# Optimization experiments

Measured on AMD Instinct MI355X. Metric: run time of the kernel, lower is better.

The kernel has to match this reference:

```python
import jax, jax.numpy as jnp
import numpy as np

NEG = -1e30       # log-space 'zero'
KD_FACTOR = 0.5   # self.kd_factor
KD_TEMP = 1.0     # self.kd_temp is never set in the original __init__; use 1.0
BLANK = 0         # torch CTCLoss default blank id


def ctc_loss(logits, targets, ilens, olens):
    """CTC negative log-likelihood, sum-reduced / B (matches builtin path:
    log_softmax + nn.CTCLoss(reduction='sum', zero_infinity=True) / batch).
    logits: [B,T,C]; targets: [B,L] label ids (no blanks); ilens, olens: [B]."""
    B, T, C = logits.shape
    L = targets.shape[1]
    S = 2 * L + 1
    lp = jax.nn.log_softmax(logits, axis=-1)                     # [B,T,C]
    # extended label sequence: blank, y1, blank, y2, ..., blank  -> [B,S]
    ext = jnp.zeros((B, S), dtype=targets.dtype).at[:, 1::2].set(targets)
    prev2 = jnp.pad(ext, ((0, 0), (2, 0)))[:, :S]
    allow2 = (ext != BLANK) & (ext != prev2) & (jnp.arange(S)[None, :] >= 2)
    # per-frame emission log-probs of extended labels: [T,B,S]
    emit = jnp.take_along_axis(lp, jnp.broadcast_to(ext[:, None, :], (B, T, S)), axis=2)
    emit = jnp.transpose(emit, (1, 0, 2))
    alpha0 = (jnp.full((B, S), NEG, dtype=lp.dtype)
              .at[:, 0].set(emit[0, :, 0])
              .at[:, 1].set(emit[0, :, 1]))

    def step(alpha, xs):
        e_t, t = xs
        s1 = jnp.pad(alpha, ((0, 0), (1, 0)), constant_values=NEG)[:, :S]
        s2 = jnp.where(allow2, jnp.pad(alpha, ((0, 0), (2, 0)), constant_values=NEG)[:, :S], NEG)
        m = jnp.maximum(jnp.maximum(alpha, s1), s2)
        new = m + jnp.log(jnp.exp(alpha - m) + jnp.exp(s1 - m) + jnp.exp(s2 - m)) + e_t
        # freeze alpha past each sample's input length -> alpha at t = ilen-1
        new = jnp.where((t < ilens)[:, None], new, alpha)
        return new, None

    alpha, _ = jax.lax.scan(step, alpha0, (emit[1:], jnp.arange(1, T)))
    end = 2 * olens                                              # last blank index
    bidx = jnp.arange(B)
    ll = jnp.logaddexp(alpha[bidx, end], alpha[bidx, end - 1])
    loss = -ll
    loss = jnp.where(loss > 1e20, 0.0, loss)                     # zero_infinity
    return loss.sum() / B


def kd_loss(logits, soft_logits, hlens):
    """Vectorized form of the per-sample ragged KD loop:
    sum_b -(softmax(soft[b,:h]/T) * log_softmax(logits[b,:h]/T)).sum() / B."""
    B, T, _ = logits.shape
    p = jax.nn.softmax(soft_logits / KD_TEMP, axis=-1)
    logq = jax.nn.log_softmax(logits / KD_TEMP, axis=-1)
    cxe = -(p * logq).sum(-1)                                    # [B,T]
    mask = jnp.arange(T)[None, :] < hlens[:, None]
    return jnp.where(mask, cxe, 0.0).sum() / B


def setup_inputs() -> dict:
    key = jax.random.key(0)
    k1, k2, k3, k4, k5, k6 = jax.random.split(key, 6)
    B, T, E, V, L = 16, 512, 512, 5000, 64
    hs_pad = jax.random.normal(k1, (B, T, E), jnp.float32)
    soft_logits = jax.random.normal(k2, (B, T, V), jnp.float32)
    W = jax.random.normal(k3, (E, V), jnp.float32) * 0.02
    b = jnp.zeros((V,), jnp.float32)
    hlens = jax.random.randint(k4, (B,), 300, T + 1)             # T >= 2L+1 guaranteed
    targets = jax.random.randint(k5, (B, L), 1, V)               # no blank labels
    olens = jax.random.randint(k6, (B,), 32, L + 1)
    return {"hs_pad": hs_pad, "soft_logits": soft_logits, "W": W, "b": b,
            "hlens": hlens, "targets": targets, "olens": olens}


def reference(hs_pad, soft_logits, W, b, hlens, targets, olens):
    # ctc_lo(F.dropout(hs_pad, p=0.0)) -> plain linear projection
    logits = hs_pad @ W + b                                      # [B,T,V]
    loss_ctc = ctc_loss(logits, targets, hlens, olens)
    loss_kd = kd_loss(logits, soft_logits, hlens)
    return KD_FACTOR * loss_kd + (1.0 - KD_FACTOR) * loss_ctc
```

## Files before the change

kernel.cpp:

```cpp
#include <hip/hip_runtime.h>
#include <math.h>

#define LOG2E 1.4426950408889634f
#define LN2 0.6931471805599453f

constexpr int B_ = 16;
constexpr int T_ = 512;
constexpr int E_ = 512;
constexpr int V_ = 5000;
constexpr int VP_ = 5120;
constexpr int CB_ = VP_ / 128;
constexpr int L_ = 64;
constexpr int S_ = 2 * L_ + 1;
constexpr int SP_ = 132;
constexpr int CLDS_STRIDE = 132;

typedef __attribute__((ext_vector_type(8))) short bf16x8;
typedef __attribute__((ext_vector_type(4))) float f32x4;

#define GLOAD_LDS16(g, l)                                                              \
  __builtin_amdgcn_global_load_lds((const __attribute__((address_space(1))) void*)(g), \
                                   (__attribute__((address_space(3))) void*)(l), 16, 0, 0)

__device__ __forceinline__ unsigned short f2bf(float x) {
  unsigned int u = __float_as_uint(x);
  unsigned int r = (u + 0x7fffu + ((u >> 16) & 1u)) >> 16;
  return (unsigned short)r;
}
__device__ __forceinline__ float bf2f(unsigned int lo16) {
  return __uint_as_float(lo16 << 16);
}

__device__ __forceinline__ float hexp2(float x) { return __builtin_amdgcn_exp2f(x); }
__device__ __forceinline__ float hlog2(float x) { return __builtin_amdgcn_logf(x); }

__device__ __forceinline__ float dpp_shr1_zero(float v) {
  int s = __float_as_int(v);
  int bc = __builtin_amdgcn_update_dpp(0, s, 0x142, 0xF, 0xF, false);
  int r = __builtin_amdgcn_update_dpp(bc, s, 0x111, 0xF, 0xF, false);
  return __int_as_float(r);
}

template <int CTRL>
__device__ __forceinline__ float dpp_mv(float v) {
  int s = __float_as_int(v);
  return __int_as_float(__builtin_amdgcn_update_dpp(s, s, CTRL, 0xF, 0xF, false));
}

__device__ __forceinline__ float blockReduceF(float v, bool is_max, volatile float* red) {
  int tid = threadIdx.x, lane = tid & 63, wid = tid >> 6;
#pragma unroll
  for (int off = 32; off > 0; off >>= 1) {
    float o = __shfl_down(v, off, 64);
    v = is_max ? fmaxf(v, o) : (v + o);
  }
  __syncthreads();
  if (lane == 0) red[wid] = v;
  __syncthreads();
  float r = red[0];
#pragma unroll
  for (int w = 1; w < 4; ++w) r = is_max ? fmaxf(r, (float)red[w]) : (r + (float)red[w]);
  return r;
}

__global__ __launch_bounds__(256) void convA(const float* __restrict__ X,
                                             unsigned short* __restrict__ Y, int n4) {
  int i = blockIdx.x * 256 + threadIdx.x;
  if (i >= n4) return;
  float4 v = ((const float4*)X)[i];
  ushort4 o;
  o.x = f2bf(v.x); o.y = f2bf(v.y); o.z = f2bf(v.z); o.w = f2bf(v.w);
  ((ushort4*)Y)[i] = o;
}

__global__ __launch_bounds__(256) void convW(const float* __restrict__ W,
                                             unsigned short* __restrict__ Wt) {
  __shared__ float tile[32][33];
  int n0 = blockIdx.x * 32, k0 = blockIdx.y * 32;
  int tid = threadIdx.x;
  int tx = tid & 31, ty = tid >> 5;
#pragma unroll
  for (int p = 0; p < 4; ++p) {
    int k = k0 + ty + p * 8, n = n0 + tx;
    tile[ty + p * 8][tx] = (n < V_) ? W[(size_t)k * V_ + n] : 0.0f;
  }
  __syncthreads();
#pragma unroll
  for (int p = 0; p < 4; ++p) {
    int n = n0 + ty + p * 8, k = k0 + tx;
    Wt[(size_t)n * E_ + k] = f2bf(tile[tx][ty + p * 8]);
  }
}

__global__ __launch_bounds__(256) void gemm_fused(const unsigned short* __restrict__ A,
                                                  const unsigned short* __restrict__ Wt,
                                                  const float* __restrict__ bias,
                                                  const float* __restrict__ soft,
                                                  const int* __restrict__ targets,
                                                  float* __restrict__ part,
                                                  float* __restrict__ lraw) {
  __shared__ __align__(16) char smem[128 * CLDS_STRIDE * 2];
  __shared__ int tgt[64];
  unsigned short* As = (unsigned short*)smem;
  unsigned short* Bs = As + 128 * 32;
  unsigned short* Clds = (unsigned short*)smem;

  int tid = threadIdx.x;
  int l = tid & 63, wid = tid >> 6;
  int lane15 = l & 15, lhalf = l >> 4;
  int wr = wid >> 1, wc = wid & 1;
  int bn = blockIdx.x * 128;
  int bm = blockIdx.y * 128;
  int bidx = bm >> 9;
  if (tid < 64) tgt[tid] = targets[bidx * L_ + tid];

  f32x4 acc[4][4] = {};

  int srow = l >> 2;
  int scol = (l & 3) * 8;
  for (int k0 = 0; k0 < E_; k0 += 32) {
#pragma unroll
    for (int i = 0; i < 2; ++i) {
      int rb = wid * 32 + i * 16;
      GLOAD_LDS16(A + (size_t)(bm + rb + srow) * E_ + k0 + scol, &As[rb * 32]);
      GLOAD_LDS16(Wt + (size_t)(bn + rb + srow) * E_ + k0 + scol, &Bs[rb * 32]);
    }
    __syncthreads();
    bf16x8 af[4], bf[4];
#pragma unroll
    for (int m = 0; m < 4; ++m)
      af[m] = *(const bf16x8*)&As[(wr * 64 + m * 16 + lane15) * 32 + lhalf * 8];
#pragma unroll
    for (int n = 0; n < 4; ++n)
      bf[n] = *(const bf16x8*)&Bs[(wc * 64 + n * 16 + lane15) * 32 + lhalf * 8];
#pragma unroll
    for (int m = 0; m < 4; ++m)
#pragma unroll
      for (int n = 0; n < 4; ++n)
        acc[m][n] = __builtin_amdgcn_mfma_f32_16x16x32_bf16(af[m], bf[n], acc[m][n], 0, 0, 0);
    __syncthreads();
  }

#pragma unroll
  for (int n = 0; n < 4; ++n) {
    int cl = wc * 64 + n * 16 + lane15;
    int col = bn + cl;
    float bv = (col < V_) ? bias[col] : 0.0f;
#pragma unroll
    for (int m = 0; m < 4; ++m) {
      int r0 = wr * 64 + m * 16 + lhalf * 4;
#pragma unroll
      for (int j = 0; j < 4; ++j)
        Clds[(r0 + j) * CLDS_STRIDE + cl] = f2bf(acc[m][n][j] + bv);
    }
  }
  __syncthreads();

  int r = tid >> 1, ch = tid & 1;
  const float* srp = soft + (size_t)(bm + r) * V_ + bn + ch * 64;
  const unsigned short* clr = Clds + r * CLDS_STRIDE + ch * 64;
  float pl = 0.f, ps = 0.f, pd = 0.f;
  if (bn + 128 <= V_) {
#pragma unroll 4
    for (int i = 0; i < 16; ++i) {
      float4 sv = *(const float4*)(srp + i * 4);
      ushort4 lv = *(const ushort4*)(clr + i * 4);
      float l0 = bf2f(lv.x), l1 = bf2f(lv.y), l2 = bf2f(lv.z), l3 = bf2f(lv.w);
      pl += hexp2(l0 * LOG2E) + hexp2(l1 * LOG2E) + hexp2(l2 * LOG2E) + hexp2(l3 * LOG2E);
      float e0 = hexp2(sv.x * LOG2E), e1 = hexp2(sv.y * LOG2E);
      float e2 = hexp2(sv.z * LOG2E), e3 = hexp2(sv.w * LOG2E);
      ps += (e0 + e1) + (e2 + e3);
      pd = fmaf(e0, l0, fmaf(e1, l1, fmaf(e2, l2, fmaf(e3, l3, pd))));
    }
  } else {
    for (int i = 0; i < 64; ++i) {
      int col = bn + ch * 64 + i;
      if (col < V_) {
        float s = srp[i];
        float lv = bf2f(clr[i]);
        pl += hexp2(lv * LOG2E);
        float e = hexp2(s * LOG2E);
        ps += e;
        pd = fmaf(e, lv, pd);
      }
    }
  }
  pl += __shfl_xor(pl, 1, 64);
  ps += __shfl_xor(ps, 1, 64);
  pd += __shfl_xor(pd, 1, 64);
  if (ch == 0) {
    float* pp = part + ((size_t)(bm + r) * CB_ + blockIdx.x) * 3;
    pp[0] = pl; pp[1] = ps; pp[2] = pd;
  }

  if (tid < 128) {
    int row = tid;
    const unsigned short* cr = Clds + row * CLDS_STRIDE;
    float* lr = lraw + (size_t)(bm + row) * SP_;
#pragma unroll 1
    for (int s = 0; s < S_; ++s) {
      int c = (s & 1) ? tgt[s >> 1] : 0;
      int cc = c - bn;
      if (cc >= 0 && cc < 128) lr[s] = bf2f(cr[cc]);
    }
  }
}

__global__ __launch_bounds__(256) void finalize(const float* __restrict__ part,
                                                const float* __restrict__ lraw,
                                                const int* __restrict__ hlens,
                                                float* __restrict__ cxe,
                                                float* __restrict__ emit) {
  int row = blockIdx.x * 4 + (threadIdx.x >> 6);
  int l = threadIdx.x & 63;
  int bidx = row >> 9, t = row & (T_ - 1);
  const float* pp = part + (size_t)row * CB_ * 3;
  float sl = 0.f, ss = 0.f, sd = 0.f;
  if (l < CB_) { sl = pp[l * 3]; ss = pp[l * 3 + 1]; sd = pp[l * 3 + 2]; }
#pragma unroll
  for (int off = 32; off > 0; off >>= 1) {
    sl += __shfl_xor(sl, off, 64);
    ss += __shfl_xor(ss, off, 64);
    sd += __shfl_xor(sd, off, 64);
  }
  float lse = hlog2(sl) * LN2;
  if (l == 0) cxe[row] = (t < hlens[bidx]) ? (lse - sd / ss) : 0.0f;

  const float* lr = lraw + (size_t)row * SP_;
  float e0 = (lr[l] - lse) * LOG2E;
  float e1 = (lr[l + 64] - lse) * LOG2E;
  float e2 = (l == 0) ? (lr[128] - lse) * LOG2E : -3e38f;
  float m = fmaxf(fmaxf(e0, e1), e2);
#pragma unroll
  for (int off = 32; off > 0; off >>= 1) m = fmaxf(m, __shfl_xor(m, off, 64));
  float* er = emit + (size_t)row * SP_;
  er[l] = hexp2(e0 - m);
  er[l + 64] = hexp2(e1 - m);
  if (l == 0) {
    er[128] = hexp2(e2 - m);
    er[130] = m;
  }
}

__device__ __forceinline__ void pstep(float& a0, float& a1, float& a2, float allowf,
                                      float e0, float e1, float e2) {
  float ua1 = dpp_shr1_zero(a1);
  float n0 = (a0 + ua1) * e0;
  float n1 = fmaf(ua1, allowf, a0 + a1) * e1;
  float n2 = (a2 + a1) * e2;
  a0 = n0; a1 = n1; a2 = n2;
}

__device__ __forceinline__ void renorm(float& a0, float& a1, float& a2, float& shift,
                                       int lane) {
  float m = fmaxf(a0, a1);
  m = (lane == 63) ? fmaxf(m, a2) : m;
  m = fmaxf(m, dpp_mv<0xB1>(m));
  m = fmaxf(m, dpp_mv<0x4E>(m));
  m = fmaxf(m, dpp_mv<0x124>(m));
  m = fmaxf(m, dpp_mv<0x128>(m));
  m = fmaxf(m, __shfl_xor(m, 16, 64));
  m = fmaxf(m, __shfl_xor(m, 32, 64));
  m = fmaxf(m, 1e-35f);
  float rs = __builtin_amdgcn_rcpf(m) * 281474976710656.0f;
  a0 *= rs; a1 *= rs; a2 *= rs;
  shift -= hlog2(rs);
}

__global__ __launch_bounds__(64) void ctc_fwd(const float* __restrict__ emit,
                                              const int* __restrict__ hlens,
                                              const int* __restrict__ targets,
                                              const int* __restrict__ olens,
                                              float* __restrict__ ctc_out) {
  int b = blockIdx.x;
  int l = threadIdx.x;
  const float* Eb = emit + (size_t)b * T_ * SP_;
  float allowf = 0.f;
  if (l >= 1) allowf = (targets[b * L_ + l] != targets[b * L_ + l - 1]) ? 1.0f : 0.0f;

  float a0, a1, a2, shift;
  {
    float2 e01 = *(const float2*)(Eb + 2 * l);
    float4 x = *(const float4*)(Eb + 128);
    a0 = (l == 0) ? e01.x : 0.0f;
    a1 = (l == 0) ? e01.y : 0.0f;
    a2 = 0.0f;
    shift = x.z;
  }
  int ilen = hlens[b];

#define LDE(tt) (*(const float2*)(Eb + (size_t)(tt) * SP_ + 2 * l))
#define LDX(tt) (*(const float4*)(Eb + (size_t)(tt) * SP_ + 128))

  float2 c0 = LDE(1), c1 = LDE(2), c2 = LDE(3), c3 = LDE(4);
  float2 c4 = LDE(5), c5 = LDE(6), c6 = LDE(7), c7 = LDE(8);
  float4 x0 = LDX(1), x1 = LDX(2), x2 = LDX(3), x3 = LDX(4);
  float4 x4 = LDX(5), x5 = LDX(6), x6 = LDX(7), x7 = LDX(8);

  int t = 1;
  for (; t + 7 <= ilen - 1; t += 8) {
    float2 p0 = LDE(t + 8), p1 = LDE(t + 9), p2 = LDE(t + 10), p3 = LDE(t + 11);
    float2 p4 = LDE(t + 12), p5 = LDE(t + 13), p6 = LDE(t + 14), p7 = LDE(t + 15);
    float4 q0 = LDX(t + 8), q1 = LDX(t + 9), q2 = LDX(t + 10), q3 = LDX(t + 11);
    float4 q4 = LDX(t + 12), q5 = LDX(t + 13), q6 = LDX(t + 14), q7 = LDX(t + 15);
    pstep(a0, a1, a2, allowf, c0.x, c0.y, x0.x);
    pstep(a0, a1, a2, allowf, c1.x, c1.y, x1.x);
    pstep(a0, a1, a2, allowf, c2.x, c2.y, x2.x);
    pstep(a0, a1, a2, allowf, c3.x, c3.y, x3.x);
    pstep(a0, a1, a2, allowf, c4.x, c4.y, x4.x);
    pstep(a0, a1, a2, allowf, c5.x, c5.y, x5.x);
    pstep(a0, a1, a2, allowf, c6.x, c6.y, x6.x);
    pstep(a0, a1, a2, allowf, c7.x, c7.y, x7.x);
    shift += ((x0.z + x1.z) + (x2.z + x3.z)) + ((x4.z + x5.z) + (x6.z + x7.z));
    renorm(a0, a1, a2, shift, l);
    c0 = p0; c1 = p1; c2 = p2; c3 = p3; c4 = p4; c5 = p5; c6 = p6; c7 = p7;
    x0 = q0; x1 = q1; x2 = q2; x3 = q3; x4 = q4; x5 = q5; x6 = q6; x7 = q7;
  }
  int rem = ilen - t;
  if (rem > 0) { pstep(a0, a1, a2, allowf, c0.x, c0.y, x0.x); shift += x0.z; }
  if (rem > 1) { pstep(a0, a1, a2, allowf, c1.x, c1.y, x1.x); shift += x1.z; }
  if (rem > 2) { pstep(a0, a1, a2, allowf, c2.x, c2.y, x2.x); shift += x2.z; }
  if (rem > 3) { pstep(a0, a1, a2, allowf, c3.x, c3.y, x3.x); shift += x3.z; }
  if (rem > 4) { pstep(a0, a1, a2, allowf, c4.x, c4.y, x4.x); shift += x4.z; }
  if (rem > 5) { pstep(a0, a1, a2, allowf, c5.x, c5.y, x5.x); shift += x5.z; }
  if (rem > 6) { pstep(a0, a1, a2, allowf, c6.x, c6.y, x6.x); shift += x6.z; }
#undef LDE
#undef LDX

  int end = 2 * olens[b];
  float aE = (end == 128) ? __shfl(a2, 63, 64) : __shfl(a0, end >> 1, 64);
  float aE1 = __shfl(a1, (end >> 1) - 1, 64);
  if (l == 0) {
    float p = aE + aE1;
    float ll = (hlog2(p) + shift) * LN2;
    float loss = -ll;
    if (!(loss <= 1e20f)) loss = 0.0f;
    ctc_out[b] = loss;
  }
}

__global__ __launch_bounds__(256) void final_reduce(const float* __restrict__ cxe,
                                                    const float* __restrict__ ctco,
                                                    float* __restrict__ out) {
  __shared__ float red[4];
  float s = 0.f;
  for (int i = threadIdx.x; i < B_ * T_; i += 256) s += cxe[i];
  s = blockReduceF(s, false, red);
  if (threadIdx.x == 0) {
    float c = 0.f;
    for (int b = 0; b < B_; ++b) c += ctco[b];
    out[0] = 0.5f * (s / (float)B_) + 0.5f * (c / (float)B_);
  }
}

extern "C" void kernel_launch(void* const* d_in, const int* in_sizes, int n_in,
                              void* d_out, int out_size, void* d_ws, size_t ws_size,
                              hipStream_t stream) {
  const float* hs = (const float*)d_in[0];
  const float* soft = (const float*)d_in[1];
  const float* W = (const float*)d_in[2];
  const float* bias = (const float*)d_in[3];
  const int* hlens = (const int*)d_in[4];
  const int* targets = (const int*)d_in[5];
  const int* olens = (const int*)d_in[6];
  float* out = (float*)d_out;

  int total = B_ * T_;
  size_t emit_n = (size_t)(total + 16) * SP_;
  float* emit = (float*)d_ws;
  float* cxe = emit + emit_n;
  float* ctco = cxe + (size_t)total;
  unsigned short* Abf = (unsigned short*)(ctco + 16);
  unsigned short* Wt = Abf + (size_t)total * E_;
  float* lraw = (float*)(Wt + (size_t)VP_ * E_);
  float* part = lraw + (size_t)total * SP_;

  dim3 blk(256);
  {
    int n4 = total * E_ / 4;
    hipLaunchKernelGGL(convA, dim3((n4 + 255) / 256), blk, 0, stream, hs, Abf, n4);
    hipLaunchKernelGGL(convW, dim3(VP_ / 32, E_ / 32), blk, 0, stream, W, Wt);
  }

  hipLaunchKernelGGL(gemm_fused, dim3(CB_, total / 128), blk, 0, stream, Abf, Wt, bias,
                     soft, targets, part, lraw);
  hipLaunchKernelGGL(finalize, dim3(total / 4), blk, 0, stream, part, lraw, hlens, cxe, emit);
  hipLaunchKernelGGL(ctc_fwd, dim3(B_), dim3(64), 0, stream, emit, hlens, targets, olens, ctco);
  hipLaunchKernelGGL(final_reduce, dim3(1), blk, 0, stream, cxe, ctco, out);
}
```

Before: 186.9 us.

## Split emission gather into a gathered-weight GEMM and drop the LDS logits epilogue

The fused GEMM no longer stages the bf16 logits tile in LDS. It computes the KD partial sums (exp-sum of logits, exp-sum of soft logits, and their dot product) straight from the MFMA accumulator registers, reducing across 16 lanes with shuffles. Partials are written per 64-column half-block, so finalize now reduces twice as many entries. CTC emission logits come from a new small GEMM against per-sample gathered weight rows (blank plus targets), prepared by a new prep kernel. This removes the serial 129-step per-row gather loop, the LDS round trip and its barrier, and the bf16 rounding of the emission logits. The cost is two extra launches, a redundant small GEMM, and uncoalesced strided reads of soft logits in the epilogue.

```diff
diff --git a/kernel.cpp b/kernel.cpp
--- a/kernel.cpp
+++ b/kernel.cpp
@@ -10,10 +10,11 @@
 constexpr int V_ = 5000;
 constexpr int VP_ = 5120;
 constexpr int CB_ = VP_ / 128;
+constexpr int CB2_ = CB_ * 2;
 constexpr int L_ = 64;
 constexpr int S_ = 2 * L_ + 1;
 constexpr int SP_ = 132;
-constexpr int CLDS_STRIDE = 132;
+constexpr int ELW_ = 80;
 
 typedef __attribute__((ext_vector_type(8))) short bf16x8;
 typedef __attribute__((ext_vector_type(4))) float f32x4;
@@ -92,27 +93,32 @@
   }
 }
 
-__global__ __launch_bounds__(256) void gemm_fused(const unsigned short* __restrict__ A,
-                                                  const unsigned short* __restrict__ Wt,
-                                                  const float* __restrict__ bias,
-                                                  const float* __restrict__ soft,
-                                                  const int* __restrict__ targets,
-                                                  float* __restrict__ part,
-                                                  float* __restrict__ lraw) {
-  __shared__ __align__(16) char smem[128 * CLDS_STRIDE * 2];
-  __shared__ int tgt[64];
-  unsigned short* As = (unsigned short*)smem;
-  unsigned short* Bs = As + 128 * 32;
-  unsigned short* Clds = (unsigned short*)smem;
-
+__global__ __launch_bounds__(256) void prep_wext(const unsigned short* __restrict__ Wt,
+                                                 const int* __restrict__ targets,
+                                                 unsigned short* __restrict__ Wext) {
+  int b = blockIdx.x;
+  int tid = threadIdx.x;
+  for (int idx = tid; idx < 65 * 128; idx += 256) {
+    int slot = idx >> 7, grp = idx & 127;
+    int c = (slot == 0) ? 0 : targets[b * L_ + slot - 1];
+    ushort4 v = *(const ushort4*)(Wt + (size_t)c * E_ + grp * 4);
+    *(ushort4*)(Wext + ((size_t)b * ELW_ + slot) * E_ + grp * 4) = v;
+  }
+}
+
+__global__ __launch_bounds__(256) void gemm_kd(const unsigned short* __restrict__ A,
+                                               const unsigned short* __restrict__ Wt,
+                                               const float* __restrict__ bias,
+                                               const float* __restrict__ soft,
+                                               float* __restrict__ part) {
+  __shared__ unsigned short As[128 * 32];
+  __shared__ unsigned short Bs[128 * 32];
   int tid = threadIdx.x;
   int l = tid & 63, wid = tid >> 6;
   int lane15 = l & 15, lhalf = l >> 4;
   int wr = wid >> 1, wc = wid & 1;
   int bn = blockIdx.x * 128;
   int bm = blockIdx.y * 128;
-  int bidx = bm >> 9;
-  if (tid < 64) tgt[tid] = targets[bidx * L_ + tid];
 
   f32x4 acc[4][4] = {};
 
@@ -141,82 +147,116 @@
     __syncthreads();
   }
 
+  int colbase = bn + wc * 64 + lane15;
+  float bv[4], validf[4];
 #pragma unroll
   for (int n = 0; n < 4; ++n) {
-    int cl = wc * 64 + n * 16 + lane15;
-    int col = bn + cl;
-    float bv = (col < V_) ? bias[col] : 0.0f;
-#pragma unroll
-    for (int m = 0; m < 4; ++m) {
-      int r0 = wr * 64 + m * 16 + lhalf * 4;
-#pragma unroll
-      for (int j = 0; j < 4; ++j)
-        Clds[(r0 + j) * CLDS_STRIDE + cl] = f2bf(acc[m][n][j] + bv);
-    }
-  }
-  __syncthreads();
-
-  int r = tid >> 1, ch = tid & 1;
-  const float* srp = soft + (size_t)(bm + r) * V_ + bn + ch * 64;
-  const unsigned short* clr = Clds + r * CLDS_STRIDE + ch * 64;
-  float pl = 0.f, ps = 0.f, pd = 0.f;
-  if (bn + 128 <= V_) {
-#pragma unroll 4
-    for (int i = 0; i < 16; ++i) {
-      float4 sv = *(const float4*)(srp + i * 4);
-      ushort4 lv = *(const ushort4*)(clr + i * 4);
-      float l0 = bf2f(lv.x), l1 = bf2f(lv.y), l2 = bf2f(lv.z), l3 = bf2f(lv.w);
-      pl += hexp2(l0 * LOG2E) + hexp2(l1 * LOG2E) + hexp2(l2 * LOG2E) + hexp2(l3 * LOG2E);
-      float e0 = hexp2(sv.x * LOG2E), e1 = hexp2(sv.y * LOG2E);
-      float e2 = hexp2(sv.z * LOG2E), e3 = hexp2(sv.w * LOG2E);
-      ps += (e0 + e1) + (e2 + e3);
-      pd = fmaf(e0, l0, fmaf(e1, l1, fmaf(e2, l2, fmaf(e3, l3, pd))));
-    }
-  } else {
-    for (int i = 0; i < 64; ++i) {
-      int col = bn + ch * 64 + i;
-      if (col < V_) {
-        float s = srp[i];
-        float lv = bf2f(clr[i]);
-        pl += hexp2(lv * LOG2E);
-        float e = hexp2(s * LOG2E);
-        ps += e;
-        pd = fmaf(e, lv, pd);
+    int col = colbase + n * 16;
+    bool v = col < V_;
+    validf[n] = v ? 1.0f : 0.0f;
+    bv[n] = v ? bias[col] : 0.0f;
+  }
+  int cb2 = blockIdx.x * 2 + wc;
+#pragma unroll
+  for (int m = 0; m < 4; ++m) {
+#pragma unroll
+    for (int j = 0; j < 4; ++j) {
+      int row = bm + wr * 64 + m * 16 + lhalf * 4 + j;
+      const float* sp = soft + (size_t)row * V_ + colbase;
+      float pl = 0.f, ps = 0.f, pd = 0.f;
+#pragma unroll
+      for (int n = 0; n < 4; ++n) {
+        float lv = acc[m][n][j] + bv[n];
+        float el = hexp2(lv * LOG2E) * validf[n];
+        float s = (validf[n] != 0.0f) ? sp[n * 16] : 0.0f;
+        float es = hexp2(s * LOG2E) * validf[n];
+        pl += el;
+        ps += es;
+        pd = fmaf(es, lv, pd);
+      }
+#pragma unroll
+      for (int off = 1; off < 16; off <<= 1) {
+        pl += __shfl_xor(pl, off, 64);
+        ps += __shfl_xor(ps, off, 64);
+        pd += __shfl_xor(pd, off, 64);
+      }
+      if (lane15 == 0) {
+        float* pp = part + ((size_t)row * CB2_ + cb2) * 3;
+        pp[0] = pl; pp[1] = ps; pp[2] = pd;
       }
     }
   }
-  pl += __shfl_xor(pl, 1, 64);
-  ps += __shfl_xor(ps, 1, 64);
-  pd += __shfl_xor(pd, 1, 64);
-  if (ch == 0) {
-    float* pp = part + ((size_t)(bm + r) * CB_ + blockIdx.x) * 3;
-    pp[0] = pl; pp[1] = ps; pp[2] = pd;
-  }
-
-  if (tid < 128) {
-    int row = tid;
-    const unsigned short* cr = Clds + row * CLDS_STRIDE;
-    float* lr = lraw + (size_t)(bm + row) * SP_;
-#pragma unroll 1
-    for (int s = 0; s < S_; ++s) {
-      int c = (s & 1) ? tgt[s >> 1] : 0;
-      int cc = c - bn;
-      if (cc >= 0 && cc < 128) lr[s] = bf2f(cr[cc]);
+}
+
+__global__ __launch_bounds__(256) void gemm_emit(const unsigned short* __restrict__ A,
+                                                 const unsigned short* __restrict__ Wext,
+                                                 const float* __restrict__ bias,
+                                                 const int* __restrict__ targets,
+                                                 float* __restrict__ EL) {
+  __shared__ unsigned short As[128 * 32];
+  int tid = threadIdx.x;
+  int l = tid & 63, wid = tid >> 6;
+  int lane15 = l & 15, lhalf = l >> 4;
+  int bm = blockIdx.x * 128;
+  int bidx = bm >> 9;
+  const unsigned short* Wb = Wext + (size_t)bidx * ELW_ * E_;
+
+  f32x4 acc[2][5] = {};
+  int srow = l >> 2, scol = (l & 3) * 8;
+  for (int k0 = 0; k0 < E_; k0 += 32) {
+#pragma unroll
+    for (int i = 0; i < 2; ++i) {
+      int rb = wid * 32 + i * 16;
+      GLOAD_LDS16(A + (size_t)(bm + rb + srow) * E_ + k0 + scol, &As[rb * 32]);
     }
-  }
+    __syncthreads();
+    bf16x8 af[2], bf[5];
+#pragma unroll
+    for (int m = 0; m < 2; ++m)
+      af[m] = *(const bf16x8*)&As[(wid * 32 + m * 16 + lane15) * 32 + lhalf * 8];
+#pragma unroll
+    for (int n = 0; n < 5; ++n)
+      bf[n] = *(const bf16x8*)(Wb + (size_t)(n * 16 + lane15) * E_ + k0 + lhalf * 8);
+#pragma unroll
+    for (int m = 0; m < 2; ++m)
+#pragma unroll
+      for (int n = 0; n < 5; ++n)
+        acc[m][n] = __builtin_amdgcn_mfma_f32_16x16x32_bf16(af[m], bf[n], acc[m][n], 0, 0, 0);
+    __syncthreads();
+  }
+  float bvE[5];
+#pragma unroll
+  for (int n = 0; n < 5; ++n) {
+    int slot = n * 16 + lane15;
+    int c = (slot == 0 || slot >= 65) ? 0 : targets[bidx * L_ + slot - 1];
+    bvE[n] = bias[c];
+  }
+#pragma unroll
+  for (int m = 0; m < 2; ++m)
+#pragma unroll
+    for (int n = 0; n < 5; ++n) {
+      int slot = n * 16 + lane15;
+#pragma unroll
+      for (int j = 0; j < 4; ++j) {
+        int row = bm + wid * 32 + m * 16 + lhalf * 4 + j;
+        EL[(size_t)row * ELW_ + slot] = acc[m][n][j] + bvE[n];
+      }
+    }
 }
 
 __global__ __launch_bounds__(256) void finalize(const float* __restrict__ part,
-                                                const float* __restrict__ lraw,
+                                                const float* __restrict__ EL,
                                                 const int* __restrict__ hlens,
                                                 float* __restrict__ cxe,
                                                 float* __restrict__ emit) {
   int row = blockIdx.x * 4 + (threadIdx.x >> 6);
   int l = threadIdx.x & 63;
   int bidx = row >> 9, t = row & (T_ - 1);
-  const float* pp = part + (size_t)row * CB_ * 3;
+  const float* pp = part + (size_t)row * CB2_ * 3;
   float sl = 0.f, ss = 0.f, sd = 0.f;
-  if (l < CB_) { sl = pp[l * 3]; ss = pp[l * 3 + 1]; sd = pp[l * 3 + 2]; }
+  for (int idx = l; idx < CB2_; idx += 64) {
+    sl += pp[idx * 3]; ss += pp[idx * 3 + 1]; sd += pp[idx * 3 + 2];
+  }
 #pragma unroll
   for (int off = 32; off > 0; off >>= 1) {
     sl += __shfl_xor(sl, off, 64);
@@ -226,10 +266,12 @@
   float lse = hlog2(sl) * LN2;
   if (l == 0) cxe[row] = (t < hlens[bidx]) ? (lse - sd / ss) : 0.0f;
 
-  const float* lr = lraw + (size_t)row * SP_;
-  float e0 = (lr[l] - lse) * LOG2E;
-  float e1 = (lr[l + 64] - lse) * LOG2E;
-  float e2 = (l == 0) ? (lr[128] - lse) * LOG2E : -3e38f;
+  const float* elr = EL + (size_t)row * ELW_;
+  int slot0 = (l & 1) ? (l >> 1) + 1 : 0;
+  int slot1 = (l & 1) ? (l >> 1) + 33 : 0;
+  float e0 = (elr[slot0] - lse) * LOG2E;
+  float e1 = (elr[slot1] - lse) * LOG2E;
+  float e2 = (l == 0) ? (elr[0] - lse) * LOG2E : -3e38f;
   float m = fmaxf(fmaxf(e0, e1), e2);
 #pragma unroll
   for (int off = 32; off > 0; off >>= 1) m = fmaxf(m, __shfl_xor(m, off, 64));
@@ -372,19 +414,23 @@
   float* ctco = cxe + (size_t)total;
   unsigned short* Abf = (unsigned short*)(ctco + 16);
   unsigned short* Wt = Abf + (size_t)total * E_;
-  float* lraw = (float*)(Wt + (size_t)VP_ * E_);
-  float* part = lraw + (size_t)total * SP_;
+  unsigned short* Wext = Wt + (size_t)VP_ * E_;
+  float* EL = (float*)(Wext + (size_t)B_ * ELW_ * E_);
+  float* part = EL + (size_t)total * ELW_;
 
   dim3 blk(256);
   {
     int n4 = total * E_ / 4;
     hipLaunchKernelGGL(convA, dim3((n4 + 255) / 256), blk, 0, stream, hs, Abf, n4);
     hipLaunchKernelGGL(convW, dim3(VP_ / 32, E_ / 32), blk, 0, stream, W, Wt);
-  }
-
-  hipLaunchKernelGGL(gemm_fused, dim3(CB_, total / 128), blk, 0, stream, Abf, Wt, bias,
-                     soft, targets, part, lraw);
-  hipLaunchKernelGGL(finalize, dim3(total / 4), blk, 0, stream, part, lraw, hlens, cxe, emit);
+    hipLaunchKernelGGL(prep_wext, dim3(B_), blk, 0, stream, Wt, targets, Wext);
+  }
+
+  hipLaunchKernelGGL(gemm_kd, dim3(CB_, total / 128), blk, 0, stream, Abf, Wt, bias,
+                     soft, part);
+  hipLaunchKernelGGL(gemm_emit, dim3(total / 128), blk, 0, stream, Abf, Wext, bias,
+                     targets, EL);
+  hipLaunchKernelGGL(finalize, dim3(total / 4), blk, 0, stream, part, EL, hlens, cxe, emit);
   hipLaunchKernelGGL(ctc_fwd, dim3(B_), dim3(64), 0, stream, emit, hlens, targets, olens, ctco);
   hipLaunchKernelGGL(final_reduce, dim3(1), blk, 0, stream, cxe, ctco, out);
 }
```

New measurement: 246.8 us. 1.32x slower.
